# Optimization experiments

Measured on AMD Instinct MI355X. Metric: run time of the kernel, lower is better.

Reference implementation:

```python
import jax, jax.numpy as jnp
import numpy as np
import math

B, T, V, D, H, L = 32, 512, 16, 256, 4, 2

def _ln(x, g, b, eps=1e-5):
    m = jnp.mean(x, -1, keepdims=True)
    v = jnp.mean((x - m) ** 2, -1, keepdims=True)
    return (x - m) * jax.lax.rsqrt(v + eps) * g + b

def _grn(x, w1, b1, w2, b2, g, bn, sw=None, sb=None):
    h = jax.nn.elu(x @ w1 + b1)
    h = h @ w2 + b2
    h1, h2 = jnp.split(h, 2, axis=-1)
    h = h1 * jax.nn.sigmoid(h2)
    skip = x if sw is None else x @ sw + sb
    return _ln(h + skip, g, bn)

def setup_inputs():
    ks = iter(jax.random.split(jax.random.key(0), 64))
    s = 0.02
    def w(*shape):
        return jax.random.normal(next(ks), shape, jnp.float32) * s
    return dict(
        x=jax.random.normal(next(ks), (B, T, V), jnp.float32),
        emb_w=w(V, D), emb_b=w(V, D),
        vg_fc1_w=w(V, D, D), vg_fc1_b=w(V, D), vg_fc2_w=w(V, D, 2 * D), vg_fc2_b=w(V, 2 * D),
        vg_ln_g=jnp.ones((V, D), jnp.float32), vg_ln_b=jnp.zeros((V, D), jnp.float32),
        sel_fc1_w=w(V * D, D), sel_fc1_b=w(D), sel_fc2_w=w(D, 2 * V), sel_fc2_b=w(2 * V),
        sel_skip_w=w(V * D, V), sel_skip_b=w(V),
        sel_ln_g=jnp.ones((V,), jnp.float32), sel_ln_b=jnp.zeros((V,), jnp.float32),
        lstm_wih=w(L, 4 * D, D), lstm_whh=w(L, 4 * D, D), lstm_bih=w(L, 4 * D), lstm_bhh=w(L, 4 * D),
        pl_fc1_w=w(D, D), pl_fc1_b=w(D), pl_fc2_w=w(D, 2 * D), pl_fc2_b=w(2 * D),
        pl_ln_g=jnp.ones((D,), jnp.float32), pl_ln_b=jnp.zeros((D,), jnp.float32),
        attn_in_w=w(3 * D, D), attn_in_b=w(3 * D), attn_out_w=w(D, D), attn_out_b=w(D),
        attn_ln_g=jnp.ones((D,), jnp.float32), attn_ln_b=jnp.zeros((D,), jnp.float32),
        pa_fc1_w=w(D, D), pa_fc1_b=w(D), pa_fc2_w=w(D, 2 * D), pa_fc2_b=w(2 * D),
        pa_ln_g=jnp.ones((D,), jnp.float32), pa_ln_b=jnp.zeros((D,), jnp.float32),
        fg_fc1_w=w(D, 4 * D), fg_fc1_b=w(4 * D), fg_fc2_w=w(4 * D, 2 * D), fg_fc2_b=w(2 * D),
        fg_ln_g=jnp.ones((D,), jnp.float32), fg_ln_b=jnp.zeros((D,), jnp.float32),
    )

def reference(x, emb_w, emb_b, vg_fc1_w, vg_fc1_b, vg_fc2_w, vg_fc2_b, vg_ln_g, vg_ln_b,
              sel_fc1_w, sel_fc1_b, sel_fc2_w, sel_fc2_b, sel_skip_w, sel_skip_b, sel_ln_g, sel_ln_b,
              lstm_wih, lstm_whh, lstm_bih, lstm_bhh,
              pl_fc1_w, pl_fc1_b, pl_fc2_w, pl_fc2_b, pl_ln_g, pl_ln_b,
              attn_in_w, attn_in_b, attn_out_w, attn_out_b, attn_ln_g, attn_ln_b,
              pa_fc1_w, pa_fc1_b, pa_fc2_w, pa_fc2_b, pa_ln_g, pa_ln_b,
              fg_fc1_w, fg_fc1_b, fg_fc2_w, fg_fc2_b, fg_ln_g, fg_ln_b):
    b, t, v = x.shape
    d = emb_w.shape[1]
    # per-feature Linear(1, d) fused into one broadcasted op: [B,T,V,D]
    embedded = x[..., None] * emb_w + emb_b
    # per-variable GRNs (no skip_fc since input==output), batched over V via einsum
    h = jax.nn.elu(jnp.einsum('btvd,vdh->btvh', embedded, vg_fc1_w) + vg_fc1_b)
    h = jnp.einsum('btvh,vho->btvo', h, vg_fc2_w) + vg_fc2_b
    h1, h2 = jnp.split(h, 2, axis=-1)
    var_out = _ln(h1 * jax.nn.sigmoid(h2) + embedded, vg_ln_g, vg_ln_b)  # [B,T,V,D]
    # selection GRN over flattened variables
    flat = embedded.reshape(b, t, v * d)
    sel = _grn(flat, sel_fc1_w, sel_fc1_b, sel_fc2_w, sel_fc2_b, sel_ln_g, sel_ln_b, sel_skip_w, sel_skip_b)
    weights = jax.nn.softmax(sel, axis=-1)  # [B,T,V]
    vsn_out = jnp.einsum('btvh,btv->bth', var_out, weights)  # [B,T,D]
    # stacked LSTM (torch gate order i,f,g,o); dropout inactive at eval
    h_seq = vsn_out
    for l in range(lstm_wih.shape[0]):
        xi = jnp.einsum('btd,gd->btg', h_seq, lstm_wih[l]) + lstm_bih[l] + lstm_bhh[l]
        whh = lstm_whh[l]
        def step(carry, xt):
            hp, cp = carry
            gates = xt + hp @ whh.T
            i, f, g, o = jnp.split(gates, 4, axis=-1)
            c = jax.nn.sigmoid(f) * cp + jax.nn.sigmoid(i) * jnp.tanh(g)
            hh = jax.nn.sigmoid(o) * jnp.tanh(c)
            return (hh, c), hh
        init = (jnp.zeros((b, d), x.dtype), jnp.zeros((b, d), x.dtype))
        _, hs = jax.lax.scan(step, init, jnp.swapaxes(xi, 0, 1))
        h_seq = jnp.swapaxes(hs, 0, 1)
    lstm_filtered = _grn(h_seq + vsn_out, pl_fc1_w, pl_fc1_b, pl_fc2_w, pl_fc2_b, pl_ln_g, pl_ln_b)
    # multihead self-attention
    qkv = lstm_filtered @ attn_in_w.T + attn_in_b
    q, k, vv = jnp.split(qkv, 3, axis=-1)
    hd = d // H
    def heads(z):
        return z.reshape(b, t, H, hd).transpose(0, 2, 1, 3)
    q, k, vv = heads(q), heads(k), heads(vv)
    scale = 1.0 / math.sqrt(hd)
    att = jax.nn.softmax(jnp.einsum('bhqd,bhkd->bhqk', q, k) * scale, axis=-1)
    o = jnp.einsum('bhqk,bhkd->bhqd', att, vv).transpose(0, 2, 1, 3).reshape(b, t, d)
    o = o @ attn_out_w.T + attn_out_b
    attn_out = _ln(o + lstm_filtered, attn_ln_g, attn_ln_b)
    attn_filtered = _grn(attn_out, pa_fc1_w, pa_fc1_b, pa_fc2_w, pa_fc2_b, pa_ln_g, pa_ln_b)
    out = _grn(attn_filtered, fg_fc1_w, fg_fc1_b, fg_fc2_w, fg_fc2_b, fg_ln_g, fg_ln_b)
    return out[:, -1, :], weights
```

## Files before the change

### kernel.cpp

```cpp
#include <hip/hip_runtime.h>
#include <hip/hip_bf16.h>
#include <hip/hip_fp8.h>
#include <math.h>


#define BT 16384
#define TT 512
#define BB 32
#define VV 16
#define DD 256

typedef unsigned short ushort;
typedef unsigned int uint;
typedef unsigned long ulong_;
typedef __attribute__((ext_vector_type(8))) short short8;
typedef __attribute__((ext_vector_type(8))) unsigned short ushort8v;
typedef __attribute__((ext_vector_type(4))) float floatx4;
typedef __attribute__((ext_vector_type(8))) int int8v;

#if __has_builtin(__builtin_amdgcn_cvt_pk_fp8_f32)
#define HW_FP8_CVT 1
#endif

__device__ __forceinline__ float sigmoidf_(float x) { return 1.f / (1.f + expf(-x)); }
__device__ __forceinline__ float eluf_(float x)     { return x > 0.f ? x : expm1f(x); }
__device__ __forceinline__ float fsig(float x) {
  return __builtin_amdgcn_rcpf(1.f + __expf(-x));
}
__device__ __forceinline__ float ftanh(float x) {
  float xc = fminf(fmaxf(x, -44.f), 44.f);
  float e = __expf(-2.f * xc);
  return (1.f - e) * __builtin_amdgcn_rcpf(1.f + e);
}
__device__ __forceinline__ ushort f2bf(float f) {
  unsigned int u = __float_as_uint(f);
  unsigned int r = u + 0x7fffu + ((u >> 16) & 1u);
  return (ushort)(r >> 16);
}
__device__ __forceinline__ float bf2f(ushort b) { return __uint_as_float(((unsigned int)b) << 16); }

__device__ __forceinline__ float2 bsum256x2(float a, float b, float* red8) {
  #pragma unroll
  for (int m = 32; m > 0; m >>= 1) { a += __shfl_xor(a, m, 64); b += __shfl_xor(b, m, 64); }
  int w = threadIdx.x >> 6;
  if ((threadIdx.x & 63) == 0) { red8[w * 2] = a; red8[w * 2 + 1] = b; }
  __syncthreads();
  float ra = red8[0] + red8[2] + red8[4] + red8[6];
  float rb = red8[1] + red8[3] + red8[5] + red8[7];
  __syncthreads();
  return make_float2(ra, rb);
}

__device__ __forceinline__ float block_sum256(float v, float* red) {
  int j = threadIdx.x;
  red[j] = v; __syncthreads();
  #pragma unroll
  for (int st = 128; st > 0; st >>= 1) {
    if (j < st) red[j] += red[j + st];
    __syncthreads();
  }
  float r = red[0];
  __syncthreads();
  return r;
}

__global__ void wtT_k(const float* __restrict__ src, ushort* __restrict__ dst,
                      int K, int N, long sStride, long dStride) {
  int b = blockIdx.z;
  src += (size_t)b * sStride; dst += (size_t)b * dStride;
  __shared__ float t[32][33];
  int k0 = blockIdx.y * 32, n0 = blockIdx.x * 32;
  int tx = threadIdx.x & 31, ty = threadIdx.x >> 5;
  #pragma unroll
  for (int i = 0; i < 32; i += 8) {
    int k = k0 + ty + i, n = n0 + tx;
    t[ty + i][tx] = (k < K && n < N) ? src[(size_t)k * N + n] : 0.f;
  }
  __syncthreads();
  #pragma unroll
  for (int i = 0; i < 32; i += 8) {
    int n = n0 + ty + i, k = k0 + tx;
    if (n < N && k < K) dst[(size_t)n * K + k] = f2bf(t[tx][ty + i]);
  }
}

__global__ void cvt_k(const float* __restrict__ src, ushort* __restrict__ dst, int n) {
  int i = blockIdx.x * 256 + threadIdx.x;
  if (i < n) dst[i] = f2bf(src[i]);
}

__global__ void redw_k(const float* __restrict__ W, int ldw,
                       const float* __restrict__ ew, const float* __restrict__ eb,
                       const float* __restrict__ bias, int biasPerV,
                       float* __restrict__ R, float* __restrict__ C, int N) {
  int v = blockIdx.x;
  int n = threadIdx.x;
  if (n >= N) return;
  const float* Wb = W + (size_t)v * 256 * ldw + n;
  const float* ewv = ew + v * 256;
  const float* ebv = eb + v * 256;
  float r = 0.f, c = 0.f;
  for (int j = 0; j < 256; j++) {
    float w = Wb[(size_t)j * ldw];
    r += ewv[j] * w;
    c += ebv[j] * w;
  }
  if (biasPerV) c += bias[v * 256 + n];
  R[v * N + n] = r;
  C[v * N + n] = c;
}

__global__ __launch_bounds__(256) void sel_h_k(const float* __restrict__ x,
                                               const float* __restrict__ R1,
                                               const float* __restrict__ C1,
                                               const float* __restrict__ b1,
                                               ushort* __restrict__ selH) {
  int m = blockIdx.x, n = threadIdx.x;
  __shared__ float xs[16];
  if (n < 16) xs[n] = x[m * 16 + n];
  __syncthreads();
  float a = b1[n];
  #pragma unroll
  for (int v = 0; v < 16; v++) a += xs[v] * R1[v * 256 + n] + C1[v * 256 + n];
  selH[(size_t)m * 256 + n] = f2bf(eluf_(a));
}

__global__ void sel_skip_k(const float* __restrict__ x,
                           const float* __restrict__ Rsk, const float* __restrict__ Csk,
                           const float* __restrict__ b, float* __restrict__ selSkip) {
  int gid = blockIdx.x * 256 + threadIdx.x;
  int m = gid >> 4, n = gid & 15;
  const float* xr = x + m * 16;
  float a = b[n];
  #pragma unroll
  for (int v = 0; v < 16; v++) a += xr[v] * Rsk[v * 16 + n] + Csk[v * 16 + n];
  selSkip[gid] = a;
}

__global__ __launch_bounds__(256) void var_h_k(const float* __restrict__ x,
                                               const float* __restrict__ R,
                                               const float* __restrict__ C,
                                               int vbase, ushort* __restrict__ bufA16) {
  int m = blockIdx.x, n = threadIdx.x;
  const float* xr = x + m * 16 + vbase;
  #pragma unroll
  for (int z = 0; z < 4; z++) {
    int v = vbase + z;
    float a = xr[z] * R[v * 256 + n] + C[v * 256 + n];
    bufA16[((size_t)z * BT + m) * 256 + n] = f2bf(eluf_(a));
  }
}

__global__ void whh_pack8_k(const float* __restrict__ whh, unsigned char* __restrict__ dst) {
  int gid = blockIdx.x * 256 + threadIdx.x;
  int layer = gid >> 13;
  int rem = gid & 8191;
  int lane = rem & 63;
  int f = (rem >> 6) & 15;
  int wave = rem >> 10;
  int kt2 = f & 1, ts = (f >> 1) & 1, g = f >> 2;
  int n = g * 256 + wave * 32 + ts * 16 + (lane & 15);
  int k0 = kt2 * 128 + (lane >> 4) * 32;
  const float* src = whh + (size_t)layer * 262144 + (size_t)n * 256 + k0;
  unsigned char* d = dst + (size_t)gid * 32;
  #pragma unroll
  for (int b = 0; b < 32; b++) {
    __hip_fp8_e4m3 q(src[b] * 64.f);
    d[b] = q.__x;
  }
}

template<int ADT, int ACT, int CDT>
__global__ __launch_bounds__(256) void mgemm_k(
    const void* __restrict__ Aall, int lda, long aStride,
    const ushort* __restrict__ Ball, long bStride,
    const float* __restrict__ biasAll, long biasStride,
    void* __restrict__ Call, int ldc, long cStride,
    int K, int Nvalid,
    const float* __restrict__ embw, const float* __restrict__ embb, int xbase) {
  int z = blockIdx.z;
  const ushort* B = Ball + (size_t)z * bStride;
  const float* bias = biasAll ? biasAll + (size_t)z * biasStride : nullptr;
  int m0 = blockIdx.y * 128, n0 = blockIdx.x * 128;
  __shared__ ushort As[128][40];
  __shared__ ushort Bs[128][40];
  int tid = threadIdx.x;
  int r = tid >> 1, half = tid & 1;
  int wave = tid >> 6, lane = tid & 63;
  int wm = (wave >> 1) * 64, wn = (wave & 1) * 64;
  int lm = lane & 15, lq = lane >> 4;
  floatx4 acc[4][4];
  #pragma unroll
  for (int i = 0; i < 4; i++)
    #pragma unroll
    for (int j = 0; j < 4; j++) acc[i][j] = (floatx4)0.f;

  for (int k0 = 0; k0 < K; k0 += 32) {
    int kk = k0 + half * 16;
    {
      int gm = m0 + r;
      ushort tmp[16];
      if (ADT == 0) {
        const float* Af = (const float*)Aall + (size_t)z * aStride + (size_t)gm * lda + kk;
        #pragma unroll
        for (int q = 0; q < 4; q++) {
          float4 f = ((const float4*)Af)[q];
          tmp[q * 4 + 0] = f2bf(f.x); tmp[q * 4 + 1] = f2bf(f.y);
          tmp[q * 4 + 2] = f2bf(f.z); tmp[q * 4 + 3] = f2bf(f.w);
        }
      } else if (ADT == 1) {
        const ushort* Ab = (const ushort*)Aall + (size_t)z * aStride + (size_t)gm * lda + kk;
        *(ushort8v*)&tmp[0] = *(const ushort8v*)(Ab);
        *(ushort8v*)&tmp[8] = *(const ushort8v*)(Ab + 8);
      } else if (ADT == 2) {
        const float* xp = (const float*)Aall;
        float xv = xp[(size_t)gm * lda + xbase + z + (kk >> 8)];
        const float4* ew = (const float4*)(embw + (size_t)z * 256 + kk);
        const float4* eb = (const float4*)(embb + (size_t)z * 256 + kk);
        #pragma unroll
        for (int q = 0; q < 4; q++) {
          float4 w4 = ew[q], b4 = eb[q];
          tmp[q * 4 + 0] = f2bf(xv * w4.x + b4.x); tmp[q * 4 + 1] = f2bf(xv * w4.y + b4.y);
          tmp[q * 4 + 2] = f2bf(xv * w4.z + b4.z); tmp[q * 4 + 3] = f2bf(xv * w4.w + b4.w);
        }
      } else {
        const float* A1 = (const float*)Aall + (size_t)z * aStride + (size_t)gm * lda + kk;
        const float* A2 = embw + (size_t)z * aStride + (size_t)gm * lda + kk;
        #pragma unroll
        for (int q = 0; q < 4; q++) {
          float4 f1 = ((const float4*)A1)[q];
          float4 f2 = ((const float4*)A2)[q];
          tmp[q * 4 + 0] = f2bf(f1.x + f2.x); tmp[q * 4 + 1] = f2bf(f1.y + f2.y);
          tmp[q * 4 + 2] = f2bf(f1.z + f2.z); tmp[q * 4 + 3] = f2bf(f1.w + f2.w);
        }
      }
      *(ushort8v*)&As[r][half * 16]     = *(ushort8v*)&tmp[0];
      *(ushort8v*)&As[r][half * 16 + 8] = *(ushort8v*)&tmp[8];
    }
    {
      int gn = n0 + r;
      ushort tmp[16];
      if (gn < Nvalid) {
        const ushort* Bp = B + (size_t)gn * K + kk;
        *(ushort8v*)&tmp[0] = *(const ushort8v*)(Bp);
        *(ushort8v*)&tmp[8] = *(const ushort8v*)(Bp + 8);
      } else {
        #pragma unroll
        for (int q = 0; q < 16; q++) tmp[q] = 0;
      }
      *(ushort8v*)&Bs[r][half * 16]     = *(ushort8v*)&tmp[0];
      *(ushort8v*)&Bs[r][half * 16 + 8] = *(ushort8v*)&tmp[8];
    }
    __syncthreads();
    short8 fa[4], fb[4];
    #pragma unroll
    for (int i = 0; i < 4; i++) fa[i] = *(const short8*)&As[wm + i * 16 + lm][lq * 8];
    #pragma unroll
    for (int j = 0; j < 4; j++) fb[j] = *(const short8*)&Bs[wn + j * 16 + lm][lq * 8];
    #pragma unroll
    for (int i = 0; i < 4; i++)
      #pragma unroll
      for (int j = 0; j < 4; j++)
        acc[i][j] = __builtin_amdgcn_mfma_f32_16x16x32_bf16(fa[i], fb[j], acc[i][j], 0, 0, 0);
    __syncthreads();
  }
  #pragma unroll
  for (int j = 0; j < 4; j++) {
    int gn = n0 + wn + j * 16 + lm;
    if (gn >= Nvalid) continue;
    float bv = bias ? bias[gn] : 0.f;
    #pragma unroll
    for (int i = 0; i < 4; i++) {
      #pragma unroll
      for (int rg = 0; rg < 4; rg++) {
        int gm = m0 + wm + i * 16 + lq * 4 + rg;
        float v = acc[i][j][rg] + bv;
        if (ACT == 1) v = eluf_(v);
        if (CDT == 0) ((float*)Call + (size_t)z * cStride)[(size_t)gm * ldc + gn] = v;
        else ((ushort*)Call + (size_t)z * cStride)[(size_t)gm * ldc + gn] = f2bf(v);
      }
    }
  }
}

__global__ void sel_finish_k(const float* __restrict__ selG, const float* __restrict__ selSkip,
                             const float* __restrict__ lng, const float* __restrict__ lnb,
                             float* __restrict__ wout, int M) {
  int m = blockIdx.x * 256 + threadIdx.x;
  if (m >= M) return;
  float s[16];
  float mean = 0.f;
  #pragma unroll
  for (int i = 0; i < 16; i++) {
    float h1 = selG[m * 32 + i], h2 = selG[m * 32 + 16 + i];
    float val = h1 * sigmoidf_(h2) + selSkip[m * 16 + i];
    s[i] = val; mean += val;
  }
  mean *= (1.f / 16.f);
  float var = 0.f;
  #pragma unroll
  for (int i = 0; i < 16; i++) { float d = s[i] - mean; var += d * d; }
  var *= (1.f / 16.f);
  float inv = rsqrtf(var + 1e-5f);
  float mx = -1e30f;
  #pragma unroll
  for (int i = 0; i < 16; i++) { s[i] = (s[i] - mean) * inv * lng[i] + lnb[i]; mx = fmaxf(mx, s[i]); }
  float sum = 0.f;
  #pragma unroll
  for (int i = 0; i < 16; i++) { s[i] = expf(s[i] - mx); sum += s[i]; }
  float isum = 1.f / sum;
  #pragma unroll
  for (int i = 0; i < 16; i++) wout[m * 16 + i] = s[i] * isum;
}

__global__ __launch_bounds__(256) void var_epi4_k(
    const ushort* __restrict__ G16,
    const float* __restrict__ x, int vbase,
    const float* __restrict__ embw, const float* __restrict__ embb,
    const float* __restrict__ lng, const float* __restrict__ lnb,
    const float* __restrict__ wts, float* __restrict__ vsn, int first) {
  int m = blockIdx.x, j = threadIdx.x;
  __shared__ float red8[8];
  float accv = 0.f;
  #pragma unroll
  for (int z = 0; z < 4; z++) {
    int v = vbase + z;
    const ushort* Gp = G16 + ((size_t)z * BT + m) * 512;
    float g1 = bf2f(Gp[j]), g2 = bf2f(Gp[256 + j]);
    float e = x[m * VV + v] * embw[z * 256 + j] + embb[z * 256 + j];
    float s = g1 * sigmoidf_(g2) + e;
    float2 r = bsum256x2(s, s * s, red8);
    float mean = r.x * (1.f / 256.f);
    float var = r.y * (1.f / 256.f) - mean * mean;
    float o = (s - mean) * rsqrtf(var + 1e-5f) * lng[z * 256 + j] + lnb[z * 256 + j];
    accv += wts[m * VV + v] * o;
  }
  size_t oi = (size_t)m * 256 + j;
  if (first) vsn[oi] = accv; else vsn[oi] += accv;
}

__global__ __launch_bounds__(256) void grn_epi_k(
    const ushort* __restrict__ G, const float* __restrict__ skipA,
    const float* __restrict__ skipB,
    const float* __restrict__ lng, const float* __restrict__ lnb,
    float* __restrict__ out) {
  int m = blockIdx.x, j = threadIdx.x;
  __shared__ float red8[8];
  float g1 = bf2f(G[(size_t)m * 512 + j]), g2 = bf2f(G[(size_t)m * 512 + 256 + j]);
  float sk = skipA[(size_t)m * 256 + j];
  if (skipB) sk += skipB[(size_t)m * 256 + j];
  float s = g1 * sigmoidf_(g2) + sk;
  float2 r = bsum256x2(s, s * s, red8);
  float mean = r.x * (1.f / 256.f);
  float var = r.y * (1.f / 256.f) - mean * mean;
  out[(size_t)m * 256 + j] = (s - mean) * rsqrtf(var + 1e-5f) * lng[j] + lnb[j];
}

__global__ void add2_k(const float* __restrict__ a, const float* __restrict__ b,
                       float* __restrict__ c, int n) {
  int i = blockIdx.x * 256 + threadIdx.x;
  if (i < n) c[i] = a[i] + b[i];
}

#define DESC (1.f / 1024.f)
#define H8S 272
__global__ __launch_bounds__(512, 2) void lstm_recur_k(
    const float* __restrict__ xi,
    const unsigned char* __restrict__ wpk,
    float* __restrict__ hout,
    int T) {
  int bb = blockIdx.x;
  int tid = threadIdx.x;
  int wave = tid >> 6, lane = tid & 63;
  int lm = lane & 15, lq = lane >> 4;
  __shared__ __align__(16) unsigned char h8[2][16 * H8S];
  for (int i = tid; i < 2 * 16 * H8S / 4; i += 512) ((uint*)h8)[i] = 0;

  int8v wr[16];
  {
    const int8v* wp = (const int8v*)wpk;
    #pragma unroll
    for (int f = 0; f < 16; f++) wr[f] = wp[(wave * 16 + f) * 64 + lane];
  }
  bool act = (lq == 0);
  int jj = wave * 32 + lm;
  const float* xg = xi + (size_t)bb * T * 1024;
  float xq[8], xn[8];
  if (act) {
    #pragma unroll
    for (int g = 0; g < 4; g++) {
      xq[2 * g]     = xg[g * 256 + jj];
      xq[2 * g + 1] = xg[g * 256 + jj + 16];
    }
  }
  float cst[2] = {0.f, 0.f};
  float hbf[2][8];
  int arow = lm * H8S + lq * 32;
  __syncthreads();

  for (int t = 0; t < T; t++) {
    int cur = t & 1, nxt = cur ^ 1;
    if (act && t + 1 < T) {
      const float* xp = xg + (size_t)(t + 1) * 1024;
      #pragma unroll
      for (int g = 0; g < 4; g++) {
        xn[2 * g]     = xp[g * 256 + jj];
        xn[2 * g + 1] = xp[g * 256 + jj + 16];
      }
    }
    int8v a[2];
    #pragma unroll
    for (int kt = 0; kt < 2; kt++)
      a[kt] = *(const int8v*)&h8[cur][arow + kt * 128];
    floatx4 acc[8];
    #pragma unroll
    for (int f = 0; f < 8; f++) acc[f] = (floatx4)0.f;
    #pragma unroll
    for (int kt = 0; kt < 2; kt++)
      #pragma unroll
      for (int f = 0; f < 8; f++)
        acc[f] = __builtin_amdgcn_mfma_scale_f32_16x16x128_f8f6f4(
            a[kt], wr[f * 2 + kt], acc[f], 0, 0, 0, 0x7f7f7f7f, 0, 0x7f7f7f7f);
    if (act) {
      int tb = t & 7;
      #pragma unroll
      for (int ts = 0; ts < 2; ts++) {
        float pi = acc[0 + ts][0] * DESC + xq[0 + ts];
        float pf = acc[2 + ts][0] * DESC + xq[2 + ts];
        float pg = acc[4 + ts][0] * DESC + xq[4 + ts];
        float po = acc[6 + ts][0] * DESC + xq[6 + ts];
        float c = fsig(pf) * cst[ts] + fsig(pi) * ftanh(pg);
        cst[ts] = c;
        hbf[ts][tb] = fsig(po) * ftanh(c);
      }
#ifdef HW_FP8_CVT
      int pk = __builtin_amdgcn_cvt_pk_fp8_f32(hbf[0][tb] * 16.f, hbf[1][tb] * 16.f, 0, false);
      h8[nxt][jj]      = (unsigned char)(pk & 0xff);
      h8[nxt][jj + 16] = (unsigned char)((pk >> 8) & 0xff);
#else
      __hip_fp8_e4m3 q0(hbf[0][tb] * 16.f), q1(hbf[1][tb] * 16.f);
      h8[nxt][jj]      = q0.__x;
      h8[nxt][jj + 16] = q1.__x;
#endif
      if (tb == 7) {
        #pragma unroll
        for (int q = 0; q < 8; q++) {
          size_t base = ((size_t)(bb * T + t - 7 + q)) * 256;
          hout[base + jj]      = hbf[0][q];
          hout[base + jj + 16] = hbf[1][q];
        }
      }
      #pragma unroll
      for (int g = 0; g < 8; g++) xq[g] = xn[g];
    }
    __syncthreads();
  }
}

__global__ __launch_bounds__(256) void attn_decode_k(const float* __restrict__ qkv,
                                                     float* __restrict__ o, int T) {
  int bh = blockIdx.x; int b = bh >> 2, h = bh & 3;
  int tid = threadIdx.x;
  __shared__ float q[64];
  __shared__ float p[512];
  __shared__ float red[256];
  if (tid < 64) q[tid] = qkv[((size_t)(b * T + T - 1)) * 768 + h * 64 + tid];
  __syncthreads();
  for (int t = tid; t < 512; t += 256) {
    const float* kv = qkv + ((size_t)(b * T + t)) * 768 + 256 + h * 64;
    float s = 0.f;
    #pragma unroll 16
    for (int d = 0; d < 64; d++) s += q[d] * kv[d];
    p[t] = s * 0.125f;
  }
  __syncthreads();
  red[tid] = fmaxf(p[tid], p[tid + 256]); __syncthreads();
  for (int st = 128; st > 0; st >>= 1) { if (tid < st) red[tid] = fmaxf(red[tid], red[tid + st]); __syncthreads(); }
  float mx = red[0]; __syncthreads();
  float e0 = expf(p[tid] - mx), e1 = expf(p[tid + 256] - mx);
  red[tid] = e0 + e1; __syncthreads();
  for (int st = 128; st > 0; st >>= 1) { if (tid < st) red[tid] += red[tid + st]; __syncthreads(); }
  float inv = 1.f / red[0];
  __syncthreads();
  p[tid] = e0; p[tid + 256] = e1;
  __syncthreads();
  int d = tid & 63, grp = tid >> 6;
  float acc = 0.f;
  for (int t = grp * 128; t < grp * 128 + 128; t++)
    acc += p[t] * qkv[((size_t)(b * T + t)) * 768 + 512 + h * 64 + d];
  red[tid] = acc; __syncthreads();
  if (grp == 0)
    o[(b * 4 + h) * 64 + d] = (red[tid] + red[tid + 64] + red[tid + 128] + red[tid + 192]) * inv;
}

__global__ __launch_bounds__(256) void attn_proj_ln_k(
    const float* __restrict__ attnO, const float* __restrict__ W, const float* __restrict__ bias,
    const float* __restrict__ lstmF, const float* __restrict__ lng, const float* __restrict__ lnb,
    float* __restrict__ out, int T) {
  int bb = blockIdx.x, j = threadIdx.x;
  __shared__ float a[256];
  __shared__ float red[256];
  a[j] = attnO[bb * 256 + j];
  __syncthreads();
  float acc = bias[j];
  const float* wr = W + (size_t)j * 256;
  #pragma unroll 8
  for (int k = 0; k < 256; k += 4) {
    float4 w4 = *(const float4*)(wr + k);
    acc += a[k] * w4.x + a[k + 1] * w4.y + a[k + 2] * w4.z + a[k + 3] * w4.w;
  }
  float s = acc + lstmF[((size_t)(bb * T + T - 1)) * 256 + j];
  float mean = block_sum256(s, red) * (1.f / 256.f);
  float d = s - mean;
  float var = block_sum256(d * d, red) * (1.f / 256.f);
  out[bb * 256 + j] = d * rsqrtf(var + 1e-5f) * lng[j] + lnb[j];
}

__global__ __launch_bounds__(256) void final_grns_k(
    const float* __restrict__ ain,
    const float* __restrict__ paw1, const float* __restrict__ pab1,
    const float* __restrict__ paw2, const float* __restrict__ pab2,
    const float* __restrict__ palg, const float* __restrict__ palb,
    const float* __restrict__ fgw1, const float* __restrict__ fgb1,
    const float* __restrict__ fgw2, const float* __restrict__ fgb2,
    const float* __restrict__ fglg, const float* __restrict__ fglb,
    float* __restrict__ out) {
  int bb = blockIdx.x, j = threadIdx.x;
  __shared__ float a[256];
  __shared__ float hbuf[1024];
  __shared__ float red[256];
  a[j] = ain[bb * 256 + j];
  __syncthreads();
  float acc = pab1[j];
  for (int k = 0; k < 256; k++) acc += a[k] * paw1[k * 256 + j];
  hbuf[j] = eluf_(acc);
  __syncthreads();
  float g1 = pab2[j], g2 = pab2[256 + j];
  for (int k = 0; k < 256; k++) { float hv = hbuf[k]; g1 += hv * paw2[k * 512 + j]; g2 += hv * paw2[k * 512 + 256 + j]; }
  float s = g1 * sigmoidf_(g2) + a[j];
  float mean = block_sum256(s, red) * (1.f / 256.f);
  float d = s - mean;
  float var = block_sum256(d * d, red) * (1.f / 256.f);
  float af = d * rsqrtf(var + 1e-5f) * palg[j] + palb[j];
  __syncthreads();
  a[j] = af;
  __syncthreads();
  float hh[4];
  #pragma unroll
  for (int q = 0; q < 4; q++) {
    int jj = j + q * 256;
    float ac = fgb1[jj];
    for (int k = 0; k < 256; k++) ac += a[k] * fgw1[k * 1024 + jj];
    hh[q] = eluf_(ac);
  }
  __syncthreads();
  #pragma unroll
  for (int q = 0; q < 4; q++) hbuf[j + q * 256] = hh[q];
  __syncthreads();
  float G1 = fgb2[j], G2 = fgb2[256 + j];
  for (int k = 0; k < 1024; k++) { float hv = hbuf[k]; G1 += hv * fgw2[k * 512 + j]; G2 += hv * fgw2[k * 512 + 256 + j]; }
  float s2 = G1 * sigmoidf_(G2) + a[j];
  mean = block_sum256(s2, red) * (1.f / 256.f);
  d = s2 - mean;
  var = block_sum256(d * d, red) * (1.f / 256.f);
  out[bb * 256 + j] = d * rsqrtf(var + 1e-5f) * fglg[j] + fglb[j];
}

extern "C" void kernel_launch(void* const* d_in, const int* in_sizes, int n_in,
                              void* d_out, int out_size, void* d_ws, size_t ws_size,
                              hipStream_t stream) {
  const float* x          = (const float*)d_in[0];
  const float* emb_w      = (const float*)d_in[1];
  const float* emb_b      = (const float*)d_in[2];
  const float* vg_fc1_w   = (const float*)d_in[3];
  const float* vg_fc1_b   = (const float*)d_in[4];
  const float* vg_fc2_w   = (const float*)d_in[5];
  const float* vg_fc2_b   = (const float*)d_in[6];
  const float* vg_ln_g    = (const float*)d_in[7];
  const float* vg_ln_b    = (const float*)d_in[8];
  const float* sel_fc1_w  = (const float*)d_in[9];
  const float* sel_fc1_b  = (const float*)d_in[10];
  const float* sel_fc2_w  = (const float*)d_in[11];
  const float* sel_fc2_b  = (const float*)d_in[12];
  const float* sel_skip_w = (const float*)d_in[13];
  const float* sel_skip_b = (const float*)d_in[14];
  const float* sel_ln_g   = (const float*)d_in[15];
  const float* sel_ln_b   = (const float*)d_in[16];
  const float* lstm_wih   = (const float*)d_in[17];
  const float* lstm_whh   = (const float*)d_in[18];
  const float* lstm_bih   = (const float*)d_in[19];
  const float* lstm_bhh   = (const float*)d_in[20];
  const float* pl_fc1_w   = (const float*)d_in[21];
  const float* pl_fc1_b   = (const float*)d_in[22];
  const float* pl_fc2_w   = (const float*)d_in[23];
  const float* pl_fc2_b   = (const float*)d_in[24];
  const float* pl_ln_g    = (const float*)d_in[25];
  const float* pl_ln_b    = (const float*)d_in[26];
  const float* attn_in_w  = (const float*)d_in[27];
  const float* attn_in_b  = (const float*)d_in[28];
  const float* attn_out_w = (const float*)d_in[29];
  const float* attn_out_b = (const float*)d_in[30];
  const float* attn_ln_g  = (const float*)d_in[31];
  const float* attn_ln_b  = (const float*)d_in[32];
  const float* pa_fc1_w   = (const float*)d_in[33];
  const float* pa_fc1_b   = (const float*)d_in[34];
  const float* pa_fc2_w   = (const float*)d_in[35];
  const float* pa_fc2_b   = (const float*)d_in[36];
  const float* pa_ln_g    = (const float*)d_in[37];
  const float* pa_ln_b    = (const float*)d_in[38];
  const float* fg_fc1_w   = (const float*)d_in[39];
  const float* fg_fc1_b   = (const float*)d_in[40];
  const float* fg_fc2_w   = (const float*)d_in[41];
  const float* fg_fc2_b   = (const float*)d_in[42];
  const float* fg_ln_g    = (const float*)d_in[43];
  const float* fg_ln_b    = (const float*)d_in[44];
  (void)in_sizes; (void)n_in; (void)out_size; (void)ws_size;

  float* out     = (float*)d_out;
  float* out_wts = out + BB * DD;

  char* p = (char*)d_ws;
  ushort* wt_sel_fc2  = (ushort*)p;                 p += 8192 * 2;
  ushort* wt_var_fc2  = (ushort*)p;                 p += 2097152 * 2;
  ushort* wt_wih      = (ushort*)p;                 p += 524288 * 2;
  unsigned char* wt_whh_pk8 = (unsigned char*)p;    p += 524288;
  ushort* wt_pl_fc1   = (ushort*)p;                 p += 65536 * 2;
  ushort* wt_pl_fc2   = (ushort*)p;                 p += 131072 * 2;
  ushort* wt_attn     = (ushort*)p;                 p += 196608 * 2;
  float*  selR        = (float*)p;                  p += 4096 * 4;
  float*  selC        = (float*)p;                  p += 4096 * 4;
  float*  varR        = (float*)p;                  p += 4096 * 4;
  float*  varC        = (float*)p;                  p += 4096 * 4;
  float*  skR         = (float*)p;                  p += 256 * 4;
  float*  skC         = (float*)p;                  p += 256 * 4;
  ushort* selH        = (ushort*)p;                 p += (size_t)BT * 256 * 2;
  float*  selSkip     = (float*)p;                  p += (size_t)BT * 16 * 4;
  float*  selG        = (float*)p;                  p += (size_t)BT * 32 * 4;
  float*  vsn         = (float*)p;                  p += (size_t)BT * 256 * 4;
  float*  hseq1       = (float*)p;                  p += (size_t)BT * 256 * 4;
  float*  hseq2       = (float*)p;                  p += (size_t)BT * 256 * 4;
  float*  cbias       = (float*)p;                  p += 4096 * 4;
  float*  attnO       = (float*)p;                  p += 8192 * 4;
  float*  attnLN      = (float*)p;                  p += 8192 * 4;
  char*   R           = p;
  ushort* bufA16 = (ushort*)R;
  ushort* bufG16 = (ushort*)(R + (((size_t)32) << 20));
  float*  xi     = (float*)R;
  ushort* plH    = (ushort*)(R + (((size_t)16) << 20));
  ushort* plG    = (ushort*)(R + (((size_t)24) << 20));
  float*  lstmF  = (float*)(R + (((size_t)48) << 20));
  float*  qkv    = (float*)R;

  dim3 blk(256);

  wtT_k<<<dim3(1, 8, 1),    blk, 0, stream>>>(sel_fc2_w,  wt_sel_fc2,  256,  32,  0, 0);
  wtT_k<<<dim3(16, 8, 16),  blk, 0, stream>>>(vg_fc2_w,   wt_var_fc2,  256,  512, 131072, 131072);
  wtT_k<<<dim3(8, 8, 1),    blk, 0, stream>>>(pl_fc1_w,   wt_pl_fc1,   256,  256, 0, 0);
  wtT_k<<<dim3(16, 8, 1),   blk, 0, stream>>>(pl_fc2_w,   wt_pl_fc2,   256,  512, 0, 0);
  cvt_k<<<2048, blk, 0, stream>>>(lstm_wih,  wt_wih, 524288);
  whh_pack8_k<<<64, blk, 0, stream>>>(lstm_whh, wt_whh_pk8);
  cvt_k<<<768,  blk, 0, stream>>>(attn_in_w, wt_attn, 196608);
  add2_k<<<8, blk, 0, stream>>>(lstm_bih, lstm_bhh, cbias, 4096);
  redw_k<<<16, 256, 0, stream>>>(sel_fc1_w,  256, emb_w, emb_b, nullptr,   0, selR, selC, 256);
  redw_k<<<16, 256, 0, stream>>>(vg_fc1_w,   256, emb_w, emb_b, vg_fc1_b,  1, varR, varC, 256);
  redw_k<<<16, 64,  0, stream>>>(sel_skip_w, 16,  emb_w, emb_b, nullptr,   0, skR,  skC,  16);

  sel_h_k<<<BT, blk, 0, stream>>>(x, selR, selC, sel_fc1_b, selH);
  sel_skip_k<<<1024, blk, 0, stream>>>(x, skR, skC, sel_skip_b, selSkip);
  mgemm_k<1,0,0><<<dim3(1, 128, 1), blk, 0, stream>>>(selH, 256, 0, wt_sel_fc2, 0, sel_fc2_b, 0,
      selG, 32, 0, 256, 32, nullptr, nullptr, 0);
  sel_finish_k<<<64, blk, 0, stream>>>(selG, selSkip, sel_ln_g, sel_ln_b, out_wts, BT);

  for (int g = 0; g < 4; g++) {
    var_h_k<<<BT, blk, 0, stream>>>(x, varR, varC, g * 4, bufA16);
    mgemm_k<1,0,1><<<dim3(4, 128, 4), blk, 0, stream>>>(bufA16, 256, (long)BT * 256,
        wt_var_fc2 + (size_t)g * 4 * 131072, 131072, vg_fc2_b + g * 2048, 512,
        bufG16, 512, (long)BT * 512, 256, 512, nullptr, nullptr, 0);
    var_epi4_k<<<BT, blk, 0, stream>>>(bufG16, x, g * 4, emb_w + g * 1024, emb_b + g * 1024,
        vg_ln_g + g * 1024, vg_ln_b + g * 1024, out_wts, vsn, g == 0 ? 1 : 0);
  }

  mgemm_k<0,0,0><<<dim3(8, 128, 1), blk, 0, stream>>>(vsn, 256, 0, wt_wih, 0, cbias, 0,
      xi, 1024, 0, 256, 1024, nullptr, nullptr, 0);
  lstm_recur_k<<<32, 512, 0, stream>>>(xi, wt_whh_pk8, hseq1, TT);
  mgemm_k<0,0,0><<<dim3(8, 128, 1), blk, 0, stream>>>(hseq1, 256, 0, wt_wih + 1024 * 256, 0,
      cbias + 1024, 0, xi, 1024, 0, 256, 1024, nullptr, nullptr, 0);
  lstm_recur_k<<<32, 512, 0, stream>>>(xi, wt_whh_pk8 + 262144, hseq2, TT);

  mgemm_k<3,1,1><<<dim3(2, 128, 1), blk, 0, stream>>>(hseq2, 256, 0, wt_pl_fc1, 0, pl_fc1_b, 0,
      plH, 256, 0, 256, 256, vsn, nullptr, 0);
  mgemm_k<1,0,1><<<dim3(4, 128, 1), blk, 0, stream>>>(plH, 256, 0, wt_pl_fc2, 0, pl_fc2_b, 0,
      plG, 512, 0, 256, 512, nullptr, nullptr, 0);
  grn_epi_k<<<BT, blk, 0, stream>>>(plG, hseq2, vsn, pl_ln_g, pl_ln_b, lstmF);

  mgemm_k<0,0,0><<<dim3(6, 128, 1), blk, 0, stream>>>(lstmF, 256, 0, wt_attn, 0, attn_in_b, 0,
      qkv, 768, 0, 256, 768, nullptr, nullptr, 0);
  attn_decode_k<<<BB * 4, blk, 0, stream>>>(qkv, attnO, TT);
  attn_proj_ln_k<<<BB, blk, 0, stream>>>(attnO, attn_out_w, attn_out_b, lstmF,
                                         attn_ln_g, attn_ln_b, attnLN, TT);

  final_grns_k<<<BB, blk, 0, stream>>>(attnLN,
      pa_fc1_w, pa_fc1_b, pa_fc2_w, pa_fc2_b, pa_ln_g, pa_ln_b,
      fg_fc1_w, fg_fc1_b, fg_fc2_w, fg_fc2_b, fg_ln_g, fg_ln_b,
      out);
}
```

Measured before the change: 2.168 ms.

## Fuse variable-GRN hidden, fc2 GEMM and LN epilogue into one kernel

Replaces the per-group loop of three kernels (hidden activation write, bf16 GEMM, gated-LN epilogue) with one kernel per 64-row tile. It computes the ELU hidden on the fly into shared memory, runs MFMA over all 16 variables with the fc2 weights pre-packed into K-tile order, and does the gate, layer norm and weighted sum in registers. This removes large bf16 intermediate buffers and their global round-trips, plus 12 launches. In exchange it uses only 256 blocks with high register pressure (launch bounds 1) and a large shared B tile, so occupancy and latency hiding may be poor.

After: 2.032 ms. 6.3% less time.

```diff
diff --git a/kernel.cpp b/kernel.cpp
--- a/kernel.cpp
+++ b/kernel.cpp
@@ -137,17 +137,17 @@
   selSkip[gid] = a;
 }
 
-__global__ __launch_bounds__(256) void var_h_k(const float* __restrict__ x,
-                                               const float* __restrict__ R,
-                                               const float* __restrict__ C,
-                                               int vbase, ushort* __restrict__ bufA16) {
-  int m = blockIdx.x, n = threadIdx.x;
-  const float* xr = x + m * 16 + vbase;
-  #pragma unroll
-  for (int z = 0; z < 4; z++) {
-    int v = vbase + z;
-    float a = xr[z] * R[v * 256 + n] + C[v * 256 + n];
-    bufA16[((size_t)z * BT + m) * 256 + n] = f2bf(eluf_(a));
+__global__ void w2pack_k(const float* __restrict__ src, ushort* __restrict__ dst) {
+  int z = blockIdx.z, kt = blockIdx.y, n0 = blockIdx.x * 64;
+  __shared__ float t[32][65];
+  for (int i = threadIdx.x; i < 2048; i += 256) {
+    int r = i >> 6, c = i & 63;
+    t[r][c] = src[(size_t)z * 131072 + (size_t)(kt * 32 + r) * 512 + n0 + c];
+  }
+  __syncthreads();
+  for (int i = threadIdx.x; i < 2048; i += 256) {
+    int c = i >> 5, kk = i & 31;
+    dst[((size_t)(z * 8 + kt) * 512 + n0 + c) * 32 + kk] = f2bf(t[kk][c]);
   }
 }
 
@@ -167,6 +167,150 @@
   for (int b = 0; b < 32; b++) {
     __hip_fp8_e4m3 q(src[b] * 64.f);
     d[b] = q.__x;
+  }
+}
+
+__global__ __launch_bounds__(256, 1) void var_fused_k(
+    const float* __restrict__ x,
+    const ushort* __restrict__ w2p,
+    const float* __restrict__ fc2b,
+    const float* __restrict__ varR, const float* __restrict__ varC,
+    const float* __restrict__ embw, const float* __restrict__ embb,
+    const float* __restrict__ lng, const float* __restrict__ lnb,
+    const float* __restrict__ wts,
+    float* __restrict__ vsn) {
+  int m0 = blockIdx.x * 64;
+  int tid = threadIdx.x;
+  int wave = tid >> 6, lane = tid & 63;
+  int lm = lane & 15, lq = lane >> 4;
+  __shared__ ushort As[64][40];
+  __shared__ ushort Bs[512][40];
+  __shared__ float xs[64][17];
+  __shared__ float wss[64][17];
+  for (int i = tid; i < 64 * 16; i += 256) {
+    int m = i >> 4, v = i & 15;
+    xs[m][v]  = x[(size_t)(m0 + m) * 16 + v];
+    wss[m][v] = wts[(size_t)(m0 + m) * 16 + v];
+  }
+  floatx4 vac[16];
+  #pragma unroll
+  for (int nt = 0; nt < 16; nt++) vac[nt] = (floatx4)0.f;
+
+  int am = tid & 63;
+  int ak = (tid >> 6) * 8;
+  ushort8v pf[8];
+  {
+    const ushort8v* s0 = (const ushort8v*)w2p + (size_t)tid * 8;
+    #pragma unroll
+    for (int q = 0; q < 8; q++) pf[q] = s0[q];
+  }
+  float4 rA0 = *(const float4*)&varR[ak];
+  float4 rA1 = *(const float4*)&varR[ak + 4];
+  float4 cA0 = *(const float4*)&varC[ak];
+  float4 cA1 = *(const float4*)&varC[ak + 4];
+  __syncthreads();
+
+  for (int z = 0; z < 16; z++) {
+    floatx4 acc[32];
+    #pragma unroll
+    for (int q = 0; q < 32; q++) acc[q] = (floatx4)0.f;
+    float xv = xs[am][z];
+    for (int kt = 0; kt < 8; kt++) {
+      int bn = tid * 2;
+      *(ushort8v*)&Bs[bn][0]      = pf[0];
+      *(ushort8v*)&Bs[bn][8]      = pf[1];
+      *(ushort8v*)&Bs[bn][16]     = pf[2];
+      *(ushort8v*)&Bs[bn][24]     = pf[3];
+      *(ushort8v*)&Bs[bn + 1][0]  = pf[4];
+      *(ushort8v*)&Bs[bn + 1][8]  = pf[5];
+      *(ushort8v*)&Bs[bn + 1][16] = pf[6];
+      *(ushort8v*)&Bs[bn + 1][24] = pf[7];
+      {
+        float rr[8] = {rA0.x, rA0.y, rA0.z, rA0.w, rA1.x, rA1.y, rA1.z, rA1.w};
+        float cc[8] = {cA0.x, cA0.y, cA0.z, cA0.w, cA1.x, cA1.y, cA1.z, cA1.w};
+        ushort tmp[8];
+        #pragma unroll
+        for (int q = 0; q < 8; q++) tmp[q] = f2bf(eluf_(xv * rr[q] + cc[q]));
+        *(ushort8v*)&As[am][ak] = *(ushort8v*)tmp;
+      }
+      int nz = (kt == 7) ? z + 1 : z;
+      int nk = (kt == 7) ? 0 : kt + 1;
+      if (nz < 16) {
+        const ushort8v* sn = (const ushort8v*)w2p + (size_t)(nz * 8 + nk) * 2048 + (size_t)tid * 8;
+        #pragma unroll
+        for (int q = 0; q < 8; q++) pf[q] = sn[q];
+        int rb = nz * 256 + nk * 32 + ak;
+        rA0 = *(const float4*)&varR[rb]; rA1 = *(const float4*)&varR[rb + 4];
+        cA0 = *(const float4*)&varC[rb]; cA1 = *(const float4*)&varC[rb + 4];
+      }
+      __syncthreads();
+      short8 fa = *(const short8*)&As[wave * 16 + lm][lq * 8];
+      #pragma unroll
+      for (int nt = 0; nt < 32; nt++) {
+        short8 fb = *(const short8*)&Bs[nt * 16 + lm][lq * 8];
+        acc[nt] = __builtin_amdgcn_mfma_f32_16x16x32_bf16(fa, fb, acc[nt], 0, 0, 0);
+      }
+      __syncthreads();
+    }
+    int strip = wave * 16;
+    float xz[4], wz[4];
+    #pragma unroll
+    for (int rg = 0; rg < 4; rg++) {
+      int r4 = strip + lq * 4 + rg;
+      xz[rg] = xs[r4][z];
+      wz[rg] = wss[r4][z];
+    }
+    float sum[4] = {0.f, 0.f, 0.f, 0.f}, sq[4] = {0.f, 0.f, 0.f, 0.f};
+    #pragma unroll
+    for (int nt = 0; nt < 16; nt++) {
+      int col = nt * 16 + lm;
+      float b1 = fc2b[z * 512 + col];
+      float b2 = fc2b[z * 512 + 256 + col];
+      float ew = embw[z * 256 + col];
+      float eb = embb[z * 256 + col];
+      #pragma unroll
+      for (int rg = 0; rg < 4; rg++) {
+        float h1 = acc[nt][rg] + b1;
+        float h2 = acc[nt + 16][rg] + b2;
+        float s = h1 * fsig(h2) + (xz[rg] * ew + eb);
+        acc[nt][rg] = s;
+        sum[rg] += s; sq[rg] += s * s;
+      }
+    }
+    #pragma unroll
+    for (int rg = 0; rg < 4; rg++) {
+      #pragma unroll
+      for (int msk = 1; msk < 16; msk <<= 1) {
+        sum[rg] += __shfl_xor(sum[rg], msk, 64);
+        sq[rg]  += __shfl_xor(sq[rg],  msk, 64);
+      }
+    }
+    float mean[4], inv[4];
+    #pragma unroll
+    for (int rg = 0; rg < 4; rg++) {
+      mean[rg] = sum[rg] * (1.f / 256.f);
+      float var = sq[rg] * (1.f / 256.f) - mean[rg] * mean[rg];
+      inv[rg] = rsqrtf(var + 1e-5f);
+    }
+    #pragma unroll
+    for (int nt = 0; nt < 16; nt++) {
+      int col = nt * 16 + lm;
+      float g = lng[z * 256 + col];
+      float b = lnb[z * 256 + col];
+      #pragma unroll
+      for (int rg = 0; rg < 4; rg++) {
+        float o = (acc[nt][rg] - mean[rg]) * inv[rg] * g + b;
+        vac[nt][rg] += wz[rg] * o;
+      }
+    }
+  }
+  int strip = wave * 16;
+  #pragma unroll
+  for (int nt = 0; nt < 16; nt++) {
+    #pragma unroll
+    for (int rg = 0; rg < 4; rg++) {
+      vsn[(size_t)(m0 + strip + lq * 4 + rg) * 256 + nt * 16 + lm] = vac[nt][rg];
+    }
   }
 }
 
@@ -212,17 +356,6 @@
         const ushort* Ab = (const ushort*)Aall + (size_t)z * aStride + (size_t)gm * lda + kk;
         *(ushort8v*)&tmp[0] = *(const ushort8v*)(Ab);
         *(ushort8v*)&tmp[8] = *(const ushort8v*)(Ab + 8);
-      } else if (ADT == 2) {
-        const float* xp = (const float*)Aall;
-        float xv = xp[(size_t)gm * lda + xbase + z + (kk >> 8)];
-        const float4* ew = (const float4*)(embw + (size_t)z * 256 + kk);
-        const float4* eb = (const float4*)(embb + (size_t)z * 256 + kk);
-        #pragma unroll
-        for (int q = 0; q < 4; q++) {
-          float4 w4 = ew[q], b4 = eb[q];
-          tmp[q * 4 + 0] = f2bf(xv * w4.x + b4.x); tmp[q * 4 + 1] = f2bf(xv * w4.y + b4.y);
-          tmp[q * 4 + 2] = f2bf(xv * w4.z + b4.z); tmp[q * 4 + 3] = f2bf(xv * w4.w + b4.w);
-        }
       } else {
         const float* A1 = (const float*)Aall + (size_t)z * aStride + (size_t)gm * lda + kk;
         const float* A2 = embw + (size_t)z * aStride + (size_t)gm * lda + kk;
@@ -311,32 +444,6 @@
   float isum = 1.f / sum;
   #pragma unroll
   for (int i = 0; i < 16; i++) wout[m * 16 + i] = s[i] * isum;
-}
-
-__global__ __launch_bounds__(256) void var_epi4_k(
-    const ushort* __restrict__ G16,
-    const float* __restrict__ x, int vbase,
-    const float* __restrict__ embw, const float* __restrict__ embb,
-    const float* __restrict__ lng, const float* __restrict__ lnb,
-    const float* __restrict__ wts, float* __restrict__ vsn, int first) {
-  int m = blockIdx.x, j = threadIdx.x;
-  __shared__ float red8[8];
-  float accv = 0.f;
-  #pragma unroll
-  for (int z = 0; z < 4; z++) {
-    int v = vbase + z;
-    const ushort* Gp = G16 + ((size_t)z * BT + m) * 512;
-    float g1 = bf2f(Gp[j]), g2 = bf2f(Gp[256 + j]);
-    float e = x[m * VV + v] * embw[z * 256 + j] + embb[z * 256 + j];
-    float s = g1 * sigmoidf_(g2) + e;
-    float2 r = bsum256x2(s, s * s, red8);
-    float mean = r.x * (1.f / 256.f);
-    float var = r.y * (1.f / 256.f) - mean * mean;
-    float o = (s - mean) * rsqrtf(var + 1e-5f) * lng[z * 256 + j] + lnb[z * 256 + j];
-    accv += wts[m * VV + v] * o;
-  }
-  size_t oi = (size_t)m * 256 + j;
-  if (first) vsn[oi] = accv; else vsn[oi] += accv;
 }
 
 __global__ __launch_bounds__(256) void grn_epi_k(
@@ -621,7 +728,7 @@
 
   char* p = (char*)d_ws;
   ushort* wt_sel_fc2  = (ushort*)p;                 p += 8192 * 2;
-  ushort* wt_var_fc2  = (ushort*)p;                 p += 2097152 * 2;
+  ushort* wt_var_fc2p = (ushort*)p;                 p += 2097152 * 2;
   ushort* wt_wih      = (ushort*)p;                 p += 524288 * 2;
   unsigned char* wt_whh_pk8 = (unsigned char*)p;    p += 524288;
   ushort* wt_pl_fc1   = (ushort*)p;                 p += 65536 * 2;
@@ -643,8 +750,6 @@
   float*  attnO       = (float*)p;                  p += 8192 * 4;
   float*  attnLN      = (float*)p;                  p += 8192 * 4;
   char*   R           = p;
-  ushort* bufA16 = (ushort*)R;
-  ushort* bufG16 = (ushort*)(R + (((size_t)32) << 20));
   float*  xi     = (float*)R;
   ushort* plH    = (ushort*)(R + (((size_t)16) << 20));
   ushort* plG    = (ushort*)(R + (((size_t)24) << 20));
@@ -654,7 +759,7 @@
   dim3 blk(256);
 
   wtT_k<<<dim3(1, 8, 1),    blk, 0, stream>>>(sel_fc2_w,  wt_sel_fc2,  256,  32,  0, 0);
-  wtT_k<<<dim3(16, 8, 16),  blk, 0, stream>>>(vg_fc2_w,   wt_var_fc2,  256,  512, 131072, 131072);
+  w2pack_k<<<dim3(8, 8, 16), blk, 0, stream>>>(vg_fc2_w, wt_var_fc2p);
   wtT_k<<<dim3(8, 8, 1),    blk, 0, stream>>>(pl_fc1_w,   wt_pl_fc1,   256,  256, 0, 0);
   wtT_k<<<dim3(16, 8, 1),   blk, 0, stream>>>(pl_fc2_w,   wt_pl_fc2,   256,  512, 0, 0);
   cvt_k<<<2048, blk, 0, stream>>>(lstm_wih,  wt_wih, 524288);
@@ -671,14 +776,8 @@
       selG, 32, 0, 256, 32, nullptr, nullptr, 0);
   sel_finish_k<<<64, blk, 0, stream>>>(selG, selSkip, sel_ln_g, sel_ln_b, out_wts, BT);
 
-  for (int g = 0; g < 4; g++) {
-    var_h_k<<<BT, blk, 0, stream>>>(x, varR, varC, g * 4, bufA16);
-    mgemm_k<1,0,1><<<dim3(4, 128, 4), blk, 0, stream>>>(bufA16, 256, (long)BT * 256,
-        wt_var_fc2 + (size_t)g * 4 * 131072, 131072, vg_fc2_b + g * 2048, 512,
-        bufG16, 512, (long)BT * 512, 256, 512, nullptr, nullptr, 0);
-    var_epi4_k<<<BT, blk, 0, stream>>>(bufG16, x, g * 4, emb_w + g * 1024, emb_b + g * 1024,
-        vg_ln_g + g * 1024, vg_ln_b + g * 1024, out_wts, vsn, g == 0 ? 1 : 0);
-  }
+  var_fused_k<<<BT / 64, blk, 0, stream>>>(x, wt_var_fc2p, vg_fc2_b, varR, varC,
+      emb_w, emb_b, vg_ln_g, vg_ln_b, out_wts, vsn);
 
   mgemm_k<0,0,0><<<dim3(8, 128, 1), blk, 0, stream>>>(vsn, 256, 0, wt_wih, 0, cbias, 0,
       xi, 1024, 0, 256, 1024, nullptr, nullptr, 0);
```
